# Kernel optimization log

Measured on AMD Instinct MI355X. Metric: run time of the kernel, lower is better.

The kernel has to match this reference:

```python
import jax, jax.numpy as jnp
import numpy as np

SIZE = 768
INNER = 64

def setup_inputs() -> dict:
    key = jax.random.key(0)
    ks = jax.random.split(key, 7)
    emb_input = jax.random.normal(ks[0], (8, 2048, SIZE), dtype=jnp.float32)
    s = 1.0 / np.sqrt(SIZE)
    Wq = jax.random.normal(ks[1], (INNER, SIZE), dtype=jnp.float32) * s
    bq = jax.random.normal(ks[2], (INNER,), dtype=jnp.float32) * 0.01
    Wk = jax.random.normal(ks[3], (INNER, SIZE), dtype=jnp.float32) * s
    bk = jax.random.normal(ks[4], (INNER,), dtype=jnp.float32) * 0.01
    Wv = jax.random.normal(ks[5], (INNER, SIZE), dtype=jnp.float32) * s
    bv = jax.random.normal(ks[6], (INNER,), dtype=jnp.float32) * 0.01
    return {"emb_input": emb_input, "Wq": Wq, "bq": bq, "Wk": Wk, "bk": bk, "Wv": Wv, "bv": bv}

def reference(emb_input, Wq, bq, Wk, bk, Wv, bv):
    # q,k,v: (B,S,inner)
    q = jnp.einsum('bse,ie->bsi', emb_input, Wq) + bq
    k = jnp.einsum('bse,ie->bsi', emb_input, Wk) + bk
    v = jnp.einsum('bse,ie->bsi', emb_input, Wv) + bv
    # NOTE: original scales by sqrt(emb_size), not sqrt(inner_size)
    scale = 1.0 / np.sqrt(SIZE).astype(np.float32)
    attn = jnp.einsum('bqi,bki->bqk', q, k) * scale  # (B,S,S)
    attn = jax.nn.softmax(attn, axis=2)
    # attn @ v, same math as original broadcast-mul-sum but as a matmul
    return jnp.einsum('bqk,bki->bqi', attn, v)
```

## Files before the change

kernel.cpp:

```cpp
#include <hip/hip_runtime.h>
#include <hip/hip_bf16.h>
#include <math.h>

#define B_  8
#define S_  2048
#define E_  768
#define I_  64

typedef __attribute__((ext_vector_type(4))) float f32x4;
typedef __attribute__((ext_vector_type(8))) short short8;
typedef __attribute__((ext_vector_type(4))) short short4v;

static __device__ __forceinline__ short bf16_of(float x) {
    unsigned u = __builtin_bit_cast(unsigned, x);
    u += 0x7fffu + ((u >> 16) & 1u);
    return (short)(u >> 16);
}

static __device__ __forceinline__ unsigned pk2(float lo, float hi) {
    __hip_bfloat162 h = __float22bfloat162_rn(float2{lo, hi});
    unsigned u; __builtin_memcpy(&u, &h, 4);
    return u;
}
static __device__ __forceinline__ short8 pk8(f32x4 a, f32x4 b) {
    union { unsigned u[4]; short8 s; } r;
    r.u[0] = pk2(a[0], a[1]); r.u[1] = pk2(a[2], a[3]);
    r.u[2] = pk2(b[0], b[1]); r.u[3] = pk2(b[2], b[3]);
    return r.s;
}

typedef __attribute__((address_space(1))) const void gv_t;
typedef __attribute__((address_space(3))) void lv_t;
static __device__ __forceinline__ void gload16(const void* g, void* l) {
    __builtin_amdgcn_global_load_lds((gv_t*)g, (lv_t*)l, 16, 0, 0);
}

#define BARRIER()   asm volatile("s_barrier" ::: "memory")
#define VMCNT(n)    asm volatile("s_waitcnt vmcnt(" #n ")" ::: "memory")

__global__ void wconv(const float* __restrict__ Wq, const float* __restrict__ bq,
                      const float* __restrict__ Wk, const float* __restrict__ bk,
                      const float* __restrict__ Wv, const float* __restrict__ bv,
                      short* __restrict__ Wb, float* __restrict__ bb, float qscale) {
    int r = blockIdx.x;
    const float* src; const float* bsrc; float sc;
    if (r < 64)       { src = Wq + r * E_;         bsrc = bq + r;         sc = qscale; }
    else if (r < 128) { src = Wk + (r - 64) * E_;  bsrc = bk + (r - 64);  sc = 1.0f; }
    else              { src = Wv + (r - 128) * E_; bsrc = bv + (r - 128); sc = 1.0f; }
    for (int j = threadIdx.x; j < E_; j += blockDim.x)
        Wb[r * E_ + j] = bf16_of(src[j] * sc);
    if (threadIdx.x == 0) bb[r] = bsrc[0] * sc;
}

__global__ __launch_bounds__(256) void qkv_proj(
    const float* __restrict__ emb, const short* __restrict__ Wb,
    const float* __restrict__ bb,
    short* __restrict__ qb, short* __restrict__ kb, short* __restrict__ vT)
{
    __shared__ float Af[2][32][64];
    __shared__ short Wf[2][192][64];

    const int tid = threadIdx.x, w = tid >> 6, l = tid & 63;
    const int lr = l & 15, rg = l >> 4;
    const int sm = w & 1, sc = w >> 1;
    const int m0 = blockIdx.x * 32;

    f32x4 acc[6];
#pragma unroll
    for (int t = 0; t < 6; ++t) acc[t] = (f32x4){0.f, 0.f, 0.f, 0.f};

    auto STAGE = [&](int ks, int d) {
        char* ab = (char*)&Af[d][0][0] + w * 2048;
#pragma unroll
        for (int i = 0; i < 2; ++i) {
            int r = w * 8 + i * 4 + (l >> 4);
            const float* src = emb + (size_t)(m0 + r) * E_ + ks * 64 + (((l & 15) ^ (r & 15)) << 2);
            gload16(src, ab + i * 1024);
        }
        char* wb2 = (char*)&Wf[d][0][0] + w * 6144;
#pragma unroll
        for (int i = 0; i < 6; ++i) {
            int r = w * 48 + i * 8 + (l >> 3);
            const short* src = Wb + (size_t)r * E_ + ks * 64 + (((l & 7) ^ (r & 7)) << 3);
            gload16(src, wb2 + i * 1024);
        }
    };

    STAGE(0, 0);
    STAGE(1, 1);

    for (int ks = 0; ks < 12; ++ks) {
        const int cur = ks & 1;
        if (ks == 11) { VMCNT(0); } else { VMCNT(8); }
        BARRIER();
#pragma unroll
        for (int h = 0; h < 2; ++h) {
            const int r = sm * 16 + lr;
            const int s0 = (h * 8 + rg * 2) ^ lr;
            const int s1 = (h * 8 + rg * 2 + 1) ^ lr;
            f32x4 a0 = *(const f32x4*)&Af[cur][r][s0 * 4];
            f32x4 a1 = *(const f32x4*)&Af[cur][r][s1 * 4];
            short8 af = pk8(a0, a1);
#pragma unroll
            for (int tt = 0; tt < 6; ++tt) {
                int rw = (sc * 6 + tt) * 16 + lr;
                short8 wf = *(const short8*)&Wf[cur][rw][((h * 4 + rg) ^ (lr & 7)) << 3];
                acc[tt] = __builtin_amdgcn_mfma_f32_16x16x32_bf16(af, wf, acc[tt], 0, 0, 0);
            }
        }
        BARRIER();
        if (ks + 2 < 12) STAGE(ks + 2, cur);
    }

#pragma unroll
    for (int tt = 0; tt < 6; ++tt) {
        int col = sc * 96 + tt * 16 + lr;
        float bias = bb[col];
        int row = m0 + sm * 16 + rg * 4;
        if (col < 64) {
#pragma unroll
            for (int j = 0; j < 4; ++j)
                qb[(size_t)(row + j) * 64 + col] = bf16_of(acc[tt][j] + bias);
        } else if (col < 128) {
#pragma unroll
            for (int j = 0; j < 4; ++j)
                kb[(size_t)(row + j) * 64 + (col - 64)] = bf16_of(acc[tt][j] + bias);
        } else {
            short4v pv;
#pragma unroll
            for (int j = 0; j < 4; ++j) pv[j] = bf16_of(acc[tt][j] + bias);
            int b = row >> 11, s = row & 2047;
            *(short4v*)&vT[((size_t)b * 64 + (col - 128)) * S_ + s] = pv;
        }
    }
}

__global__ __launch_bounds__(256) void flash_attn(
    const short* __restrict__ qb, const short* __restrict__ kb,
    const short* __restrict__ vT, float* __restrict__ out)
{
    __shared__ __align__(16) char smem[81920];
    short (*Kb)[2][64][64] = (short(*)[2][64][64])(smem);
    short (*Vb)[2][64][64] = (short(*)[2][64][64])(smem + 32768);
    short (*plds)[32][64]  = (short(*)[32][64]) (smem + 65536);
    float (*mbuf)[64][32]  = (float(*)[64][32])(smem);
    float (*rsb)[32]       = (float(*)[32])    (smem + 16384);

    const int tid = threadIdx.x, w = tid >> 6, l = tid & 63;
    const int lr = l & 15, rg = l >> 4;
    const int g = w & 1, c = w >> 1;
    const int batch = blockIdx.x & 7;
    const int qt = blockIdx.x >> 3;
    const int qloc0 = qt * 64 + g * 32;

    const short* kbB = kb + (size_t)batch * S_ * 64;
    const short* vTB = vT + (size_t)batch * 64 * S_;

    const int swsrc = ((l & 7) ^ (l >> 3)) << 3;
    auto STAGE = [&](int ks, int d) {
        const int kt = c * 16 + ks;
        const int rl = g * 32 + (l >> 3);
        char* kd = (char*)&Kb[c][d][0][0] + g * 4096;
        char* vd = (char*)&Vb[c][d][0][0] + g * 4096;
#pragma unroll
        for (int i = 0; i < 4; ++i) {
            gload16(kbB + (size_t)(kt * 64 + rl + i * 8) * 64 + swsrc, kd + i * 1024);
            gload16(vTB + (size_t)(rl + i * 8) * S_ + kt * 64 + swsrc, vd + i * 1024);
        }
    };

    short8 aq[2][2];
#pragma unroll
    for (int mg = 0; mg < 2; ++mg)
#pragma unroll
        for (int h = 0; h < 2; ++h)
            aq[mg][h] = *(const short8*)(qb + (size_t)(batch * S_ + qloc0 + mg * 16 + lr) * 64 + h * 32 + rg * 8);

    f32x4 acc[2][4];
    float rs[2][4];
#pragma unroll
    for (int mg = 0; mg < 2; ++mg)
#pragma unroll
        for (int n = 0; n < 4; ++n) { acc[mg][n] = (f32x4){0.f, 0.f, 0.f, 0.f}; rs[mg][n] = 0.f; }

    STAGE(0, 0);
    STAGE(1, 1);

    for (int ks = 0; ks < 16; ++ks) {
        const int cur = ks & 1;
        if (ks == 15) { VMCNT(0); } else { VMCNT(8); }
        BARRIER();

        f32x4 s2[2][4];
#pragma unroll
        for (int t = 0; t < 4; ++t) {
            const int rk = t * 16 + lr;
            short8 kf0 = *(const short8*)&Kb[c][cur][rk][((0 * 4 + rg) ^ (lr & 7)) << 3];
            short8 kf1 = *(const short8*)&Kb[c][cur][rk][((1 * 4 + rg) ^ (lr & 7)) << 3];
#pragma unroll
            for (int mg = 0; mg < 2; ++mg) {
                f32x4 z = (f32x4){0.f, 0.f, 0.f, 0.f};
                z = __builtin_amdgcn_mfma_f32_16x16x32_bf16(aq[mg][0], kf0, z, 0, 0, 0);
                s2[mg][t] = __builtin_amdgcn_mfma_f32_16x16x32_bf16(aq[mg][1], kf1, z, 0, 0, 0);
            }
        }
        short8 pa[2][2];
#pragma unroll
        for (int mg = 0; mg < 2; ++mg) {
            short* pb = &plds[w][mg * 16][0];
#pragma unroll
            for (int t = 0; t < 4; ++t) {
                float p0 = __builtin_amdgcn_exp2f(s2[mg][t][0]);
                float p1 = __builtin_amdgcn_exp2f(s2[mg][t][1]);
                float p2 = __builtin_amdgcn_exp2f(s2[mg][t][2]);
                float p3 = __builtin_amdgcn_exp2f(s2[mg][t][3]);
                rs[mg][0] += p0; rs[mg][1] += p1; rs[mg][2] += p2; rs[mg][3] += p3;
                unsigned w0 = pk2(p0, p1), w1 = pk2(p2, p3);
                const int sl = t * 2 + (lr >> 3), bi = lr & 7;
                pb[(rg * 4 + 0) * 64 + ((sl ^ ((rg * 4 + 0) & 7)) << 3) + bi] = (short)w0;
                pb[(rg * 4 + 1) * 64 + ((sl ^ ((rg * 4 + 1) & 7)) << 3) + bi] = (short)(w0 >> 16);
                pb[(rg * 4 + 2) * 64 + ((sl ^ ((rg * 4 + 2) & 7)) << 3) + bi] = (short)w1;
                pb[(rg * 4 + 3) * 64 + ((sl ^ ((rg * 4 + 3) & 7)) << 3) + bi] = (short)(w1 >> 16);
            }
            pa[mg][0] = *(const short8*)&pb[lr * 64 + (((0 * 4 + rg) ^ (lr & 7)) << 3)];
            pa[mg][1] = *(const short8*)&pb[lr * 64 + (((1 * 4 + rg) ^ (lr & 7)) << 3)];
        }
#pragma unroll
        for (int n = 0; n < 4; ++n) {
            const int ri = n * 16 + lr;
            short8 v0 = *(const short8*)&Vb[c][cur][ri][((0 * 4 + rg) ^ (lr & 7)) << 3];
            short8 v1 = *(const short8*)&Vb[c][cur][ri][((1 * 4 + rg) ^ (lr & 7)) << 3];
#pragma unroll
            for (int mg = 0; mg < 2; ++mg) {
                acc[mg][n] = __builtin_amdgcn_mfma_f32_16x16x32_bf16(pa[mg][0], v0, acc[mg][n], 0, 0, 0);
                acc[mg][n] = __builtin_amdgcn_mfma_f32_16x16x32_bf16(pa[mg][1], v1, acc[mg][n], 0, 0, 0);
            }
        }

        BARRIER();
        if (ks + 2 < 16) STAGE(ks + 2, cur);
    }

#pragma unroll
    for (int mg = 0; mg < 2; ++mg)
#pragma unroll
        for (int m = 1; m < 16; m <<= 1)
#pragma unroll
            for (int j = 0; j < 4; ++j) rs[mg][j] += __shfl_xor(rs[mg][j], m, 64);

    if (c == 1) {
#pragma unroll
        for (int mg = 0; mg < 2; ++mg) {
#pragma unroll
            for (int n = 0; n < 4; ++n)
#pragma unroll
                for (int j = 0; j < 4; ++j) mbuf[g][l][mg * 16 + n * 4 + j] = acc[mg][n][j];
            if (lr == 0) {
#pragma unroll
                for (int j = 0; j < 4; ++j) rsb[g][mg * 16 + rg * 4 + j] = rs[mg][j];
            }
        }
    }
    __syncthreads();
    if (c == 0) {
#pragma unroll
        for (int mg = 0; mg < 2; ++mg) {
            const int qrow = batch * S_ + qloc0 + mg * 16 + rg * 4;
#pragma unroll
            for (int j = 0; j < 4; ++j) {
                float inv = 1.0f / (rs[mg][j] + rsb[g][mg * 16 + rg * 4 + j]);
                float* orow = out + (size_t)(qrow + j) * 64;
#pragma unroll
                for (int n = 0; n < 4; ++n)
                    orow[n * 16 + lr] = (acc[mg][n][j] + mbuf[g][l][mg * 16 + n * 4 + j]) * inv;
            }
        }
    }
}

extern "C" void kernel_launch(void* const* d_in, const int* in_sizes, int n_in,
                              void* d_out, int out_size, void* d_ws, size_t ws_size,
                              hipStream_t stream) {
    const float* emb = (const float*)d_in[0];
    const float* Wq  = (const float*)d_in[1];
    const float* bq  = (const float*)d_in[2];
    const float* Wk  = (const float*)d_in[3];
    const float* bk  = (const float*)d_in[4];
    const float* Wv  = (const float*)d_in[5];
    const float* bv  = (const float*)d_in[6];
    float* out = (float*)d_out;

    char* ws = (char*)d_ws;
    short* Wb  = (short*)(ws + 0);
    float* bb  = (float*)(ws + 294912);
    short* qb  = (short*)(ws + 295680);
    short* kb  = (short*)(ws + 295680 + 2097152);
    short* vT  = (short*)(ws + 295680 + 2 * 2097152);

    const float qscale = 1.4426950408889634f / sqrtf((float)E_);

    hipLaunchKernelGGL(wconv, dim3(192), dim3(256), 0, stream,
                       Wq, bq, Wk, bk, Wv, bv, Wb, bb, qscale);
    hipLaunchKernelGGL(qkv_proj, dim3(512), dim3(256), 0, stream,
                       emb, Wb, bb, qb, kb, vT);
    hipLaunchKernelGGL(flash_attn, dim3(256), dim3(256), 0, stream,
                       qb, kb, vT, out);
}
```

Baseline: 47.00 us.

## Split attention key range across four wave pairs with 512-thread blocks

Doubles the flash-attention block to 512 threads so four wave pairs each handle a quarter of the key sequence, using 32-key stages. Swapping the QK^T MFMA operand order puts P in a transposed layout, so each lane writes one packed uint2 per tile instead of scattered 16-bit stores, and the row-sum reduction shrinks to two shuffles. Partial outputs and sums from three wave pairs go through LDS and are merged by the first pair. This should raise the wave count and shorten the serial key loop, at the cost of a larger cross-wave reduction, more LDS traffic, and tighter register limits under the 512-thread launch bound.

```diff
diff --git a/kernel.cpp b/kernel.cpp
--- a/kernel.cpp
+++ b/kernel.cpp
@@ -135,16 +135,16 @@
     }
 }
 
-__global__ __launch_bounds__(256) void flash_attn(
+__global__ __launch_bounds__(512) void flash_attn(
     const short* __restrict__ qb, const short* __restrict__ kb,
     const short* __restrict__ vT, float* __restrict__ out)
 {
     __shared__ __align__(16) char smem[81920];
-    short (*Kb)[2][64][64] = (short(*)[2][64][64])(smem);
-    short (*Vb)[2][64][64] = (short(*)[2][64][64])(smem + 32768);
-    short (*plds)[32][64]  = (short(*)[32][64]) (smem + 65536);
-    float (*mbuf)[64][32]  = (float(*)[64][32])(smem);
-    float (*rsb)[32]       = (float(*)[32])    (smem + 16384);
+    short (*Kb)[2][32][64] = (short(*)[2][32][64])(smem);
+    short (*Vb)[2][64][32] = (short(*)[2][64][32])(smem + 32768);
+    uint2 (*pbuf)[32][8]   = (uint2(*)[32][8])  (smem + 65536);
+    float* mpart  = (float*)smem;
+    float* rspart = (float*)(smem + 49152);
 
     const int tid = threadIdx.x, w = tid >> 6, l = tid & 63;
     const int lr = l & 15, rg = l >> 4;
@@ -156,16 +156,18 @@
     const short* kbB = kb + (size_t)batch * S_ * 64;
     const short* vTB = vT + (size_t)batch * 64 * S_;
 
-    const int swsrc = ((l & 7) ^ (l >> 3)) << 3;
+    const int swk = ((l & 7) ^ (l >> 3)) << 3;
+    const int swv = (((l & 3) ^ ((l >> 3) & 3)) << 3);
     auto STAGE = [&](int ks, int d) {
-        const int kt = c * 16 + ks;
-        const int rl = g * 32 + (l >> 3);
-        char* kd = (char*)&Kb[c][d][0][0] + g * 4096;
-        char* vd = (char*)&Vb[c][d][0][0] + g * 4096;
-#pragma unroll
-        for (int i = 0; i < 4; ++i) {
-            gload16(kbB + (size_t)(kt * 64 + rl + i * 8) * 64 + swsrc, kd + i * 1024);
-            gload16(vTB + (size_t)(rl + i * 8) * S_ + kt * 64 + swsrc, vd + i * 1024);
+        const int k0 = c * 512 + ks * 32;
+#pragma unroll
+        for (int i = 0; i < 2; ++i) {
+            const int rloc = g * 16 + i * 8;
+            gload16(kbB + (size_t)(k0 + rloc + (l >> 3)) * 64 + swk,
+                    (char*)&Kb[c][d][rloc][0]);
+            const int dloc = g * 32 + i * 16;
+            gload16(vTB + (size_t)(dloc + (l >> 2)) * S_ + k0 + swv,
+                    (char*)&Vb[c][d][dloc][0]);
         }
     };
 
@@ -177,64 +179,65 @@
             aq[mg][h] = *(const short8*)(qb + (size_t)(batch * S_ + qloc0 + mg * 16 + lr) * 64 + h * 32 + rg * 8);
 
     f32x4 acc[2][4];
-    float rs[2][4];
+    float rs[2] = {0.f, 0.f};
 #pragma unroll
     for (int mg = 0; mg < 2; ++mg)
 #pragma unroll
-        for (int n = 0; n < 4; ++n) { acc[mg][n] = (f32x4){0.f, 0.f, 0.f, 0.f}; rs[mg][n] = 0.f; }
+        for (int n = 0; n < 4; ++n) acc[mg][n] = (f32x4){0.f, 0.f, 0.f, 0.f};
+
+    uint2* pwr[2][4];
+    const uint2* prd[2];
+#pragma unroll
+    for (int mg = 0; mg < 2; ++mg) {
+#pragma unroll
+        for (int t = 0; t < 2; ++t) {
+            pwr[mg][t * 2 + 0] = &pbuf[w][mg * 16 + lr][(t * 4 + rg) ^ ((lr & 3) << 1)];
+            pwr[mg][t * 2 + 1] = pwr[mg][t * 2 + 0];
+        }
+        prd[mg] = &pbuf[w][mg * 16 + lr][2 * (rg ^ (lr & 3))];
+    }
 
     STAGE(0, 0);
     STAGE(1, 1);
 
     for (int ks = 0; ks < 16; ++ks) {
         const int cur = ks & 1;
-        if (ks == 15) { VMCNT(0); } else { VMCNT(8); }
+        if (ks == 15) { VMCNT(0); } else { VMCNT(4); }
         BARRIER();
 
-        f32x4 s2[2][4];
-#pragma unroll
-        for (int t = 0; t < 4; ++t) {
+        f32x4 s2[2][2];
+#pragma unroll
+        for (int t = 0; t < 2; ++t) {
             const int rk = t * 16 + lr;
             short8 kf0 = *(const short8*)&Kb[c][cur][rk][((0 * 4 + rg) ^ (lr & 7)) << 3];
             short8 kf1 = *(const short8*)&Kb[c][cur][rk][((1 * 4 + rg) ^ (lr & 7)) << 3];
 #pragma unroll
             for (int mg = 0; mg < 2; ++mg) {
                 f32x4 z = (f32x4){0.f, 0.f, 0.f, 0.f};
-                z = __builtin_amdgcn_mfma_f32_16x16x32_bf16(aq[mg][0], kf0, z, 0, 0, 0);
-                s2[mg][t] = __builtin_amdgcn_mfma_f32_16x16x32_bf16(aq[mg][1], kf1, z, 0, 0, 0);
+                z = __builtin_amdgcn_mfma_f32_16x16x32_bf16(kf0, aq[mg][0], z, 0, 0, 0);
+                s2[mg][t] = __builtin_amdgcn_mfma_f32_16x16x32_bf16(kf1, aq[mg][1], z, 0, 0, 0);
             }
         }
-        short8 pa[2][2];
-#pragma unroll
-        for (int mg = 0; mg < 2; ++mg) {
-            short* pb = &plds[w][mg * 16][0];
-#pragma unroll
-            for (int t = 0; t < 4; ++t) {
+#pragma unroll
+        for (int mg = 0; mg < 2; ++mg)
+#pragma unroll
+            for (int t = 0; t < 2; ++t) {
                 float p0 = __builtin_amdgcn_exp2f(s2[mg][t][0]);
                 float p1 = __builtin_amdgcn_exp2f(s2[mg][t][1]);
                 float p2 = __builtin_amdgcn_exp2f(s2[mg][t][2]);
                 float p3 = __builtin_amdgcn_exp2f(s2[mg][t][3]);
-                rs[mg][0] += p0; rs[mg][1] += p1; rs[mg][2] += p2; rs[mg][3] += p3;
-                unsigned w0 = pk2(p0, p1), w1 = pk2(p2, p3);
-                const int sl = t * 2 + (lr >> 3), bi = lr & 7;
-                pb[(rg * 4 + 0) * 64 + ((sl ^ ((rg * 4 + 0) & 7)) << 3) + bi] = (short)w0;
-                pb[(rg * 4 + 1) * 64 + ((sl ^ ((rg * 4 + 1) & 7)) << 3) + bi] = (short)(w0 >> 16);
-                pb[(rg * 4 + 2) * 64 + ((sl ^ ((rg * 4 + 2) & 7)) << 3) + bi] = (short)w1;
-                pb[(rg * 4 + 3) * 64 + ((sl ^ ((rg * 4 + 3) & 7)) << 3) + bi] = (short)(w1 >> 16);
+                rs[mg] += (p0 + p1) + (p2 + p3);
+                *pwr[mg][t * 2] = uint2{pk2(p0, p1), pk2(p2, p3)};
             }
-            pa[mg][0] = *(const short8*)&pb[lr * 64 + (((0 * 4 + rg) ^ (lr & 7)) << 3)];
-            pa[mg][1] = *(const short8*)&pb[lr * 64 + (((1 * 4 + rg) ^ (lr & 7)) << 3)];
-        }
+        short8 pa[2];
+#pragma unroll
+        for (int mg = 0; mg < 2; ++mg) pa[mg] = *(const short8*)prd[mg];
 #pragma unroll
         for (int n = 0; n < 4; ++n) {
-            const int ri = n * 16 + lr;
-            short8 v0 = *(const short8*)&Vb[c][cur][ri][((0 * 4 + rg) ^ (lr & 7)) << 3];
-            short8 v1 = *(const short8*)&Vb[c][cur][ri][((1 * 4 + rg) ^ (lr & 7)) << 3];
-#pragma unroll
-            for (int mg = 0; mg < 2; ++mg) {
-                acc[mg][n] = __builtin_amdgcn_mfma_f32_16x16x32_bf16(pa[mg][0], v0, acc[mg][n], 0, 0, 0);
-                acc[mg][n] = __builtin_amdgcn_mfma_f32_16x16x32_bf16(pa[mg][1], v1, acc[mg][n], 0, 0, 0);
-            }
+            short8 vf = *(const short8*)&Vb[c][cur][n * 16 + lr][(rg ^ ((lr >> 1) & 3)) * 8];
+#pragma unroll
+            for (int mg = 0; mg < 2; ++mg)
+                acc[mg][n] = __builtin_amdgcn_mfma_f32_16x16x32_bf16(pa[mg], vf, acc[mg][n], 0, 0, 0);
         }
 
         BARRIER();
@@ -242,23 +245,21 @@
     }
 
 #pragma unroll
-    for (int mg = 0; mg < 2; ++mg)
-#pragma unroll
-        for (int m = 1; m < 16; m <<= 1)
-#pragma unroll
-            for (int j = 0; j < 4; ++j) rs[mg][j] += __shfl_xor(rs[mg][j], m, 64);
-
-    if (c == 1) {
+    for (int mg = 0; mg < 2; ++mg) {
+        rs[mg] += __shfl_xor(rs[mg], 16, 64);
+        rs[mg] += __shfl_xor(rs[mg], 32, 64);
+    }
+
+    if (c != 0) {
+        const int base = ((c - 1) * 2 + g) * 2048 + l * 32;
 #pragma unroll
         for (int mg = 0; mg < 2; ++mg) {
 #pragma unroll
             for (int n = 0; n < 4; ++n)
 #pragma unroll
-                for (int j = 0; j < 4; ++j) mbuf[g][l][mg * 16 + n * 4 + j] = acc[mg][n][j];
-            if (lr == 0) {
-#pragma unroll
-                for (int j = 0; j < 4; ++j) rsb[g][mg * 16 + rg * 4 + j] = rs[mg][j];
-            }
+                for (int j = 0; j < 4; ++j)
+                    mpart[base + mg * 16 + n * 4 + j] = acc[mg][n][j];
+            if (l < 16) rspart[((c - 1) * 2 + g) * 32 + mg * 16 + l] = rs[mg];
         }
     }
     __syncthreads();
@@ -268,11 +269,21 @@
             const int qrow = batch * S_ + qloc0 + mg * 16 + rg * 4;
 #pragma unroll
             for (int j = 0; j < 4; ++j) {
-                float inv = 1.0f / (rs[mg][j] + rsb[g][mg * 16 + rg * 4 + j]);
+                const int qj = rg * 4 + j;
+                float tot = __shfl(rs[mg], qj, 64);
+#pragma unroll
+                for (int cc = 0; cc < 3; ++cc)
+                    tot += rspart[(cc * 2 + g) * 32 + mg * 16 + qj];
+                float inv = 1.0f / tot;
                 float* orow = out + (size_t)(qrow + j) * 64;
 #pragma unroll
-                for (int n = 0; n < 4; ++n)
-                    orow[n * 16 + lr] = (acc[mg][n][j] + mbuf[g][l][mg * 16 + n * 4 + j]) * inv;
+                for (int n = 0; n < 4; ++n) {
+                    float v = acc[mg][n][j];
+#pragma unroll
+                    for (int cc = 0; cc < 3; ++cc)
+                        v += mpart[(cc * 2 + g) * 2048 + l * 32 + mg * 16 + n * 4 + j];
+                    orow[n * 16 + lr] = v * inv;
+                }
             }
         }
     }
@@ -303,6 +314,6 @@
                        Wq, bq, Wk, bk, Wv, bv, Wb, bb, qscale);
     hipLaunchKernelGGL(qkv_proj, dim3(512), dim3(256), 0, stream,
                        emb, Wb, bb, qb, kb, vT);
-    hipLaunchKernelGGL(flash_attn, dim3(256), dim3(256), 0, stream,
+    hipLaunchKernelGGL(flash_attn, dim3(256), dim3(512), 0, stream,
                        qb, kb, vT, out);
 }
```

Result: faster. 44.86 us (-4.6%).
